# Kernel optimization log

Hardware: AMD Instinct MI355X
Metric: run time of the kernel (lower is better)

## Reference

```python
import jax, jax.numpy as jnp
import numpy as np

NUM_HEADS = 8
ATTENTION_SPAN = 128
LOOKAHEAD = True
NEG_INF = -1e9  # tf.keras Softmax mask adder


def setup_inputs() -> dict:
    key = jax.random.key(0)
    k1, k2, k3 = jax.random.split(key, 3)
    B, S, D = 4, 2048, 512
    x = jax.random.normal(k1, (B, S, D), dtype=jnp.float32)
    w_qkv = jax.random.normal(k2, (D, 3 * D), dtype=jnp.float32) * (D ** -0.5)
    w_proj = jax.random.normal(k3, (D, D), dtype=jnp.float32) * (D ** -0.5)
    return {"x": x, "w_qkv": w_qkv, "w_proj": w_proj}


def _band_mask(S: int) -> jnp.ndarray:
    idx = jnp.arange(S)
    m = jnp.abs(idx[None, :] - idx[:, None]) <= ATTENTION_SPAN
    if not LOOKAHEAD:
        m = m & (idx[None, :] <= idx[:, None])
    return m  # [S, S] bool


def reference(x, w_qkv, w_proj):
    B, S, D = x.shape
    H = NUM_HEADS
    hd = D // H
    scale = D ** -0.5  # NOTE: source scales by full dim, not head_dim

    qkv = x @ w_qkv                                   # [B,S,3D]
    qkv = qkv.reshape(B, S, H, 3 * hd).transpose(0, 2, 1, 3)  # [B,H,S,3hd]
    q, k, v = jnp.split(qkv, 3, axis=-1)              # each [B,H,S,hd]

    scores = jnp.einsum('bhqd,bhkd->bhqk', q, k) * scale  # [B,H,S,S]
    mask = _band_mask(S)[None, None, :, :]
    scores = scores + (1.0 - mask.astype(scores.dtype)) * NEG_INF
    attn = jax.nn.softmax(scores, axis=-1)

    out = jnp.einsum('bhqk,bhkd->bhqd', attn, v)      # [B,H,S,hd]
    out = out.transpose(0, 2, 1, 3).reshape(B, S, D)
    return out @ w_proj
```

## Files before the change

kernel.cpp:

```cpp
#include <hip/hip_runtime.h>

typedef unsigned short u16;
typedef __attribute__((ext_vector_type(8))) short s16x8;
typedef __attribute__((ext_vector_type(4))) float f32x4;

#define MFMA16(a, b, c) __builtin_amdgcn_mfma_f32_16x16x32_bf16((a), (b), (c), 0, 0, 0)

__device__ __forceinline__ u16 f2bf(float f) {
  unsigned u = __float_as_uint(f);
  u += 0x7fffu + ((u >> 16) & 1u);
  return (u16)(u >> 16);
}

__device__ __forceinline__ void gld_lds16(const void* g, void* l) {
  __builtin_amdgcn_global_load_lds(
      (const __attribute__((address_space(1))) void*)g,
      (__attribute__((address_space(3))) void*)l, 16, 0, 0);
}

__global__ __launch_bounds__(256) void prep(const float* __restrict__ X,
                                            const float* __restrict__ Wqkv,
                                            const float* __restrict__ Wproj,
                                            u16* __restrict__ Xb,
                                            u16* __restrict__ wqT,
                                            u16* __restrict__ wpT) {
  const int bid = blockIdx.x;
  if (bid < 2048) {
    size_t idx = (size_t)bid * 256 + threadIdx.x;
    const float4 f0 = *(const float4*)(X + idx * 8);
    const float4 f1 = *(const float4*)(X + idx * 8 + 4);
    float fs[8] = {f0.x, f0.y, f0.z, f0.w, f1.x, f1.y, f1.z, f1.w};
    s16x8 hv;
#pragma unroll
    for (int j = 0; j < 8; ++j) hv[j] = (short)f2bf(fs[j]);
    *(s16x8*)(Xb + idx * 8) = hv;
  } else if (bid < 2432) {
    int idx = (bid - 2048) * 256 + threadIdx.x;
    int n = idx % 1536;
    int kc = idx / 1536;
    int t = n >> 9, ct = n & 511, h = ct >> 6, d = ct & 63;
    int src_c = h * 192 + t * 64 + d;
    s16x8 hv;
#pragma unroll
    for (int i = 0; i < 8; ++i) hv[i] = (short)f2bf(Wqkv[(size_t)(kc * 8 + i) * 1536 + src_c]);
    *(s16x8*)(wqT + (size_t)n * 512 + (size_t)kc * 8) = hv;
  } else {
    int idx = (bid - 2432) * 256 + threadIdx.x;
    int n = idx % 512;
    int kc = idx / 512;
    s16x8 hv;
#pragma unroll
    for (int i = 0; i < 8; ++i) hv[i] = (short)f2bf(Wproj[(size_t)(kc * 8 + i) * 512 + n]);
    *(s16x8*)(wpT + (size_t)n * 512 + (size_t)kc * 8) = hv;
  }
}

template <int EPI, int NCOL>
__global__ __launch_bounds__(256) void gemm_bf16(
    const u16* __restrict__ A, const u16* __restrict__ B,
    float* __restrict__ OUT,
    u16* __restrict__ qo, u16* __restrict__ ko, u16* __restrict__ vto) {
  __shared__ u16 LDS[EPI ? 16640 : 16384];
  u16* SA = LDS;
  u16* SB = LDS + 8192;
  const int tid = threadIdx.x;
  const int w = tid >> 6, lane = tid & 63;
  const int l15 = lane & 15, l4 = lane >> 4;
  const int bid0 = blockIdx.x;
  const int work = (bid0 & 7) * (8 * NCOL) + (bid0 >> 3);
  const int bx = work / NCOL;
  const int by = work % NCOL;
  const int row0 = bx * 128;
  const int col0 = by * 128;
  const int wr = w >> 1, wc = w & 1;

  const int lrow = lane >> 3, lslot = lane & 7;
  const int srcoff = lrow * 1024 + ((lslot ^ lrow) << 4);
  const char* pA = (const char*)A + (size_t)(row0 + w * 32) * 1024 + srcoff;
  const char* pB = (const char*)B + (size_t)(col0 + w * 32) * 1024 + srcoff;
  u16* sAw = SA + (w * 32) * 64;
  u16* sBw = SB + (w * 32) * 64;

  const f32x4 fz = {0.f, 0.f, 0.f, 0.f};
  f32x4 acc[4][4];
  for (int a = 0; a < 4; ++a)
    for (int b = 0; b < 4; ++b) acc[a][b] = fz;

  for (int t = 0; t < 8; ++t) {
    const size_t kb = (size_t)t * 128;
#pragma unroll
    for (int j = 0; j < 4; ++j) {
      gld_lds16(pA + j * 8192 + kb, sAw + j * 512);
      gld_lds16(pB + j * 8192 + kb, sBw + j * 512);
    }
    __syncthreads();
#pragma unroll
    for (int ks = 0; ks < 2; ++ks) {
      s16x8 af[4], bf[4];
#pragma unroll
      for (int mi = 0; mi < 4; ++mi) {
        const int r = wr * 64 + mi * 16 + l15;
        const int sl = (ks * 4 + l4) ^ (r & 7);
        af[mi] = *(const s16x8*)&SA[r * 64 + sl * 8];
      }
#pragma unroll
      for (int nj = 0; nj < 4; ++nj) {
        const int r = wc * 64 + nj * 16 + l15;
        const int sl = (ks * 4 + l4) ^ (r & 7);
        bf[nj] = *(const s16x8*)&SB[r * 64 + sl * 8];
      }
#pragma unroll
      for (int nj = 0; nj < 4; ++nj)
#pragma unroll
        for (int mi = 0; mi < 4; ++mi) acc[mi][nj] = MFMA16(af[mi], bf[nj], acc[mi][nj]);
    }
    __syncthreads();
  }

  if (EPI == 0) {
#pragma unroll
    for (int mi = 0; mi < 4; ++mi)
#pragma unroll
      for (int nj = 0; nj < 4; ++nj)
#pragma unroll
        for (int rg = 0; rg < 4; ++rg) {
          int r_g = row0 + wr * 64 + mi * 16 + l4 * 4 + rg;
          int c_g = col0 + wc * 64 + nj * 16 + l15;
          OUT[(size_t)r_g * 512 + c_g] = acc[mi][nj][rg];
        }
    return;
  }

  const int b = row0 >> 11, srow = row0 & 2047;
  if (by < 8) {
    const int isq = (by < 4);
    const float QS = 0.06375874f;
    u16* dst = isq ? qo : ko;
#pragma unroll
    for (int mi = 0; mi < 4; ++mi)
#pragma unroll
      for (int nj = 0; nj < 4; ++nj)
#pragma unroll
        for (int rg = 0; rg < 4; ++rg) {
          float v = acc[mi][nj][rg];
          if (isq) v *= QS;
          int s = srow + wr * 64 + mi * 16 + l4 * 4 + rg;
          int ct = ((by & 3) * 128 + wc * 64 + nj * 16 + l15);
          int h = ct >> 6, d = ct & 63;
          dst[(((size_t)b * 8 + h) * 2048 + s) * 64 + d] = f2bf(v);
        }
  } else {
#pragma unroll
    for (int mi = 0; mi < 4; ++mi)
#pragma unroll
      for (int nj = 0; nj < 4; ++nj)
#pragma unroll
        for (int rg = 0; rg < 4; ++rg) {
          int c = wc * 64 + nj * 16 + l15;
          int s = wr * 64 + mi * 16 + l4 * 4 + rg;
          LDS[c * 130 + s] = f2bf(acc[mi][nj][rg]);
        }
    __syncthreads();
    const unsigned* LDSw = (const unsigned*)LDS;
    int c = tid >> 1, sh = tid & 1;
    int ct = (by - 8) * 128 + c;
    int h = ct >> 6, d = ct & 63;
    size_t o = (((size_t)b * 8 + h) * 64 + d) * 2048 + srow + sh * 64;
    unsigned wbuf[32];
#pragma unroll
    for (int p = 0; p < 32; ++p) wbuf[p] = LDSw[c * 65 + sh * 32 + p];
#pragma unroll
    for (int j = 0; j < 8; ++j) {
      uint4 u = {wbuf[j * 4], wbuf[j * 4 + 1], wbuf[j * 4 + 2], wbuf[j * 4 + 3]};
      *(uint4*)(vto + o + j * 8) = u;
    }
  }
}

__global__ __launch_bounds__(512, 6) void attn_kernel(
    const u16* __restrict__ q, const u16* __restrict__ k,
    const u16* __restrict__ vt, u16* __restrict__ ao) {
  __shared__ u16 KT[2][64 * 64];
  __shared__ u16 VT[2][64 * 64];
  __shared__ u16 Ph[8][16 * 64];
  const int tid = threadIdx.x;
  const int w = tid >> 6, lane = tid & 63;
  const int l15 = lane & 15, l4 = lane >> 4;
  const int bid0 = blockIdx.x;
  const int bid = (bid0 & 7) * 64 + (bid0 >> 3);
  const int qt = bid & 15, hh = (bid >> 4) & 7, b = bid >> 7;
  const size_t base = (size_t)(b * 8 + hh) * 2048 * 64;
  const int q0 = qt * 128 + w * 16;

  s16x8 qf[2];
#pragma unroll
  for (int ks = 0; ks < 2; ++ks)
    qf[ks] = *(const s16x8*)(q + base + (size_t)(q0 + l15) * 64 + ks * 32 + l4 * 8);

  const f32x4 fz = {0.f, 0.f, 0.f, 0.f};
  f32x4 O[4];
  for (int nd = 0; nd < 4; ++nd) O[nd] = fz;
  float l_acc[4] = {0.f, 0.f, 0.f, 0.f};

  const int lrow = lane >> 3, lslot = lane & 7;
  const int swzb = (lslot ^ lrow) << 4;
  const char* pK = (const char*)(k + base) + (w * 8 + lrow) * 128 + swzb;
  const char* pV = (const char*)(vt + base) + (size_t)(w * 8 + lrow) * 4096 + swzb;
  u16* dK = &KT[0][0] + w * 512;
  u16* dV = &VT[0][0] + w * 512;

#define STAGE(c_, b_)                                    \
  do {                                                   \
    gld_lds16(pK + (c_) * 8192, dK + (b_) * 4096);       \
    gld_lds16(pV + (c_) * 128,  dV + (b_) * 4096);       \
  } while (0)

  const int c0 = (2 * qt - 2) < 0 ? 0 : (2 * qt - 2);
  const int c1 = (2 * qt + 3) > 31 ? 31 : (2 * qt + 3);

  STAGE(c0, 0);
  __syncthreads();

  for (int c = c0; c <= c1; ++c) {
    const int buf = (c - c0) & 1;
    if (c < c1) STAGE(c + 1, buf ^ 1);
    const int kb = c * 64;
    const bool skip = (kb - (q0 + 15) > 128) || (q0 - (kb + 63) > 128);
    if (!skip) {
      f32x4 S[4];
      for (int nj = 0; nj < 4; ++nj) S[nj] = fz;
#pragma unroll
      for (int nj = 0; nj < 4; ++nj) {
        const int r = nj * 16 + l15;
#pragma unroll
        for (int ks = 0; ks < 2; ++ks) {
          const int sl = (ks * 4 + l4) ^ (r & 7);
          s16x8 kf = *(const s16x8*)&KT[buf][r * 64 + sl * 8];
          S[nj] = MFMA16(qf[ks], kf, S[nj]);
        }
      }
      const bool needmask = (kb + 63 - q0 > 128) || (q0 + 15 - kb > 128);
#pragma unroll
      for (int nj = 0; nj < 4; ++nj)
#pragma unroll
        for (int rg = 0; rg < 4; ++rg) {
          const int row = l4 * 4 + rg;
          const int col = nj * 16 + l15;
          float p = exp2f(S[nj][rg]);
          if (needmask) {
            int dd = (kb + col) - (q0 + row);
            if (dd > 128 || dd < -128) p = 0.f;
          }
          l_acc[rg] += p;
          const int e = (((col >> 3) ^ (row & 7)) << 3) + (col & 7);
          Ph[w][row * 64 + e] = f2bf(p);
        }
#pragma unroll
      for (int ksp = 0; ksp < 2; ++ksp) {
        const int sl0 = (ksp * 4 + l4) ^ (l15 & 7);
        s16x8 pa = *(const s16x8*)&Ph[w][l15 * 64 + sl0 * 8];
#pragma unroll
        for (int nd = 0; nd < 4; ++nd) {
          const int r = nd * 16 + l15;
          const int sl = (ksp * 4 + l4) ^ (r & 7);
          s16x8 vf = *(const s16x8*)&VT[buf][r * 64 + sl * 8];
          O[nd] = MFMA16(pa, vf, O[nd]);
        }
      }
    }
    __syncthreads();
  }
#undef STAGE

#pragma unroll
  for (int rg = 0; rg < 4; ++rg) {
    float s = l_acc[rg];
    s += __shfl_xor(s, 1);
    s += __shfl_xor(s, 2);
    s += __shfl_xor(s, 4);
    s += __shfl_xor(s, 8);
    l_acc[rg] = 1.0f / s;
  }
#pragma unroll
  for (int rg = 0; rg < 4; ++rg) {
    const int s_g = q0 + l4 * 4 + rg;
#pragma unroll
    for (int nd = 0; nd < 4; ++nd) {
      float v = O[nd][rg] * l_acc[rg];
      const int c_g = hh * 64 + nd * 16 + l15;
      ao[((size_t)b * 2048 + s_g) * 512 + c_g] = f2bf(v);
    }
  }
}

extern "C" void kernel_launch(void* const* d_in, const int* in_sizes, int n_in,
                              void* d_out, int out_size, void* d_ws, size_t ws_size,
                              hipStream_t stream) {
  const float* x = (const float*)d_in[0];
  const float* wqkv = (const float*)d_in[1];
  const float* wproj = (const float*)d_in[2];
  float* out = (float*)d_out;

  char* ws = (char*)d_ws;
  size_t off = 0;
  auto alloc = [&](size_t bytes) {
    void* p = ws + off;
    off += (bytes + 255) & ~(size_t)255;
    return p;
  };
  const size_t E = (size_t)4 * 8 * 2048 * 64;
  u16* Xb  = (u16*)alloc(E * 2);
  u16* qb  = (u16*)alloc(E * 2);
  u16* kb  = (u16*)alloc(E * 2);
  u16* vtb = (u16*)alloc(E * 2);
  u16* aob = (u16*)alloc(E * 2);
  u16* wqT = (u16*)alloc((size_t)1536 * 512 * 2);
  u16* wpT = (u16*)alloc((size_t)512 * 512 * 2);

  prep<<<dim3(2560), dim3(256), 0, stream>>>(x, wqkv, wproj, Xb, wqT, wpT);
  gemm_bf16<1, 12><<<dim3(768), dim3(256), 0, stream>>>(Xb, wqT, nullptr, qb, kb, vtb);
  attn_kernel<<<dim3(512), dim3(512), 0, stream>>>(qb, kb, vtb, aob);
  gemm_bf16<0, 4><<<dim3(256), dim3(256), 0, stream>>>(aob, wpT, out, nullptr, nullptr, nullptr);
}
```

Before: 70.42 us.

## Double-buffer GEMM K-loop with 32-wide K tiles and async LDS prefetch

The GEMM main loop now uses two LDS buffers with 32-element K slices over 16 iterations instead of one 64-wide buffer over 8. The direct global-to-LDS load for the next slice is issued before the MFMAs on the current slice, so memory latency can overlap with compute. The swizzle is adjusted to the narrower row width. It keeps one barrier per iteration but does less MFMA work between barriers, and it relies on the async loads completing by that barrier.

```diff
diff --git a/kernel.cpp b/kernel.cpp
--- a/kernel.cpp
+++ b/kernel.cpp
@@ -74,48 +74,53 @@
   const int col0 = by * 128;
   const int wr = w >> 1, wc = w & 1;
 
-  const int lrow = lane >> 3, lslot = lane & 7;
-  const int srcoff = lrow * 1024 + ((lslot ^ lrow) << 4);
+  const int lrow = lane >> 2, lslot = lane & 3;
+  const int srcoff = lrow * 1024 + ((lslot ^ (lrow & 3)) << 4);
   const char* pA = (const char*)A + (size_t)(row0 + w * 32) * 1024 + srcoff;
   const char* pB = (const char*)B + (size_t)(col0 + w * 32) * 1024 + srcoff;
-  u16* sAw = SA + (w * 32) * 64;
-  u16* sBw = SB + (w * 32) * 64;
+  u16* sAw = SA + (w * 32) * 32;
+  u16* sBw = SB + (w * 32) * 32;
+
+#define STAGE(t_, b_)                                             \
+  do {                                                            \
+    const int kbb = (t_)*64;                                      \
+    gld_lds16(pA + kbb,         sAw + (b_)*4096);                 \
+    gld_lds16(pA + 16384 + kbb, sAw + (b_)*4096 + 512);           \
+    gld_lds16(pB + kbb,         sBw + (b_)*4096);                 \
+    gld_lds16(pB + 16384 + kbb, sBw + (b_)*4096 + 512);           \
+  } while (0)
 
   const f32x4 fz = {0.f, 0.f, 0.f, 0.f};
   f32x4 acc[4][4];
   for (int a = 0; a < 4; ++a)
     for (int b = 0; b < 4; ++b) acc[a][b] = fz;
 
-  for (int t = 0; t < 8; ++t) {
-    const size_t kb = (size_t)t * 128;
-#pragma unroll
-    for (int j = 0; j < 4; ++j) {
-      gld_lds16(pA + j * 8192 + kb, sAw + j * 512);
-      gld_lds16(pB + j * 8192 + kb, sBw + j * 512);
-    }
+  STAGE(0, 0);
+  __syncthreads();
+
+  for (int t = 0; t < 16; ++t) {
+    const int cur = t & 1;
+    if (t + 1 < 16) STAGE(t + 1, cur ^ 1);
+    s16x8 af[4], bf[4];
+#pragma unroll
+    for (int mi = 0; mi < 4; ++mi) {
+      const int r = wr * 64 + mi * 16 + l15;
+      const int sl = l4 ^ (r & 3);
+      af[mi] = *(const s16x8*)&SA[cur * 4096 + r * 32 + sl * 8];
+    }
+#pragma unroll
+    for (int nj = 0; nj < 4; ++nj) {
+      const int r = wc * 64 + nj * 16 + l15;
+      const int sl = l4 ^ (r & 3);
+      bf[nj] = *(const s16x8*)&SB[cur * 4096 + r * 32 + sl * 8];
+    }
+#pragma unroll
+    for (int nj = 0; nj < 4; ++nj)
+#pragma unroll
+      for (int mi = 0; mi < 4; ++mi) acc[mi][nj] = MFMA16(af[mi], bf[nj], acc[mi][nj]);
     __syncthreads();
-#pragma unroll
-    for (int ks = 0; ks < 2; ++ks) {
-      s16x8 af[4], bf[4];
-#pragma unroll
-      for (int mi = 0; mi < 4; ++mi) {
-        const int r = wr * 64 + mi * 16 + l15;
-        const int sl = (ks * 4 + l4) ^ (r & 7);
-        af[mi] = *(const s16x8*)&SA[r * 64 + sl * 8];
-      }
-#pragma unroll
-      for (int nj = 0; nj < 4; ++nj) {
-        const int r = wc * 64 + nj * 16 + l15;
-        const int sl = (ks * 4 + l4) ^ (r & 7);
-        bf[nj] = *(const s16x8*)&SB[r * 64 + sl * 8];
-      }
-#pragma unroll
-      for (int nj = 0; nj < 4; ++nj)
-#pragma unroll
-        for (int mi = 0; mi < 4; ++mi) acc[mi][nj] = MFMA16(af[mi], bf[nj], acc[mi][nj]);
-    }
-    __syncthreads();
-  }
+  }
+#undef STAGE
 
   if (EPI == 0) {
 #pragma unroll
```

New measurement: 64.93 us. 1.08x faster.
